# Kernel optimization log

Hardware: AMD Instinct MI355X
Metric: run time of the kernel (lower is better)

The kernel has to match this reference:

```python
import jax, jax.numpy as jnp
import numpy as np

B, T, D = 2, 2048, 2048
NH, NKV = 16, 4
HD = D // NH  # 128
BASE, TSL = 10000.0, 1024


def rotary_tables(T, hd, base=BASE, tsl=TSL):
    # Matches Rotary.forward with rd == hd (rd=0 in __init__ -> full head dim).
    ar = jnp.arange(0, hd, 2, dtype=jnp.float32) / hd
    if T <= tsl:
        inv = 1.0 / (base ** ar)
    else:
        # NTK-style rescale; note right-assoc exponent in original torch code:
        # 1/(base * (T/tsl) ** ((rd/(rd-2)) ** ar))
        inv = 1.0 / (base * jnp.power(T / tsl, jnp.power(hd / (hd - 2.0), ar)))
    f = jnp.outer(jnp.arange(T, dtype=jnp.float32), inv)  # [T, hd//2]
    cos = jnp.cos(f)[None, :, None, :]  # [1,T,1,hd//2]
    sin = jnp.sin(f)[None, :, None, :]
    return cos, sin


def apply_rope(x, cos, sin):
    # full-dim rope: split halves, rotate
    h = x.shape[-1] // 2
    x1, x2 = x[..., :h], x[..., h:]
    return jnp.concatenate((x1 * cos + x2 * sin, -x1 * sin + x2 * cos), axis=-1)


def rms_norm(x):
    eps = jnp.finfo(x.dtype).eps
    return x * jax.lax.rsqrt(jnp.mean(x * x, axis=-1, keepdims=True) + eps)


def setup_inputs() -> dict:
    key = jax.random.key(0)
    k0, k1, k2, k3, k4 = jax.random.split(key, 5)
    s = 0.02
    return {
        "x": jax.random.normal(k0, (B, T, D), jnp.float32),
        "qw": jax.random.normal(k1, (NH * HD, D), jnp.float32) * s,
        "kw": jax.random.normal(k2, (NKV * HD, D), jnp.float32) * s,
        "vw": jax.random.normal(k3, (NKV * HD, D), jnp.float32) * s,
        "ow": jax.random.normal(k4, (D, D), jnp.float32) * s,
        "qg": jnp.ones((NH,), jnp.float32),
    }


def reference(x, qw, kw, vw, ow, qg):
    Bx, Tx, Dx = x.shape
    q = (x @ qw.T).reshape(Bx, Tx, NH, HD)
    k = (x @ kw.T).reshape(Bx, Tx, NKV, HD)
    v = (x @ vw.T).reshape(Bx, Tx, NKV, HD)
    q = rms_norm(q)
    k = rms_norm(k)
    cos, sin = rotary_tables(Tx, HD)
    q = apply_rope(q, cos, sin) * qg[None, None, :, None]
    k = apply_rope(k, cos, sin)
    # GQA: repeat kv heads
    r = NH // NKV
    k = jnp.repeat(k, r, axis=2)  # [B,T,NH,HD]
    v = jnp.repeat(v, r, axis=2)
    scale = 1.0 / jnp.sqrt(jnp.asarray(HD, q.dtype))
    scores = jnp.einsum("bqhd,bkhd->bhqk", q, k) * scale  # [B,NH,T,T]
    causal = jnp.tril(jnp.ones((Tx, Tx), dtype=bool))
    scores = jnp.where(causal[None, None, :, :], scores, jnp.asarray(-jnp.inf, scores.dtype))
    attn = jax.nn.softmax(scores, axis=-1)
    y = jnp.einsum("bhqk,bkhd->bqhd", attn, v)  # [B,T,NH,HD]
    return y.reshape(Bx, Tx, Dx) @ ow.T
```

## Files before the change

kernel.cpp:

```cpp
#include <hip/hip_runtime.h>
#include <hip/hip_bf16.h>
#include <stdint.h>


typedef __attribute__((ext_vector_type(8))) short short8;
typedef __attribute__((ext_vector_type(4))) float f32x4;
typedef __attribute__((ext_vector_type(16))) float f32x16;

#define GLOAD16(gp, lp) \
  __builtin_amdgcn_global_load_lds((const __attribute__((address_space(1))) void*)(gp), \
                                   (__attribute__((address_space(3))) void*)(lp), 16, 0, 0)

#define BAR() do { asm volatile("" ::: "memory"); __builtin_amdgcn_s_barrier(); asm volatile("" ::: "memory"); } while (0)

__device__ __forceinline__ float bf2f(unsigned short u) {
  union { unsigned int i; float f; } v; v.i = ((unsigned int)u) << 16; return v.f;
}
__device__ __forceinline__ unsigned short f2bf(float f) {
  union { float fl; unsigned int i; } v; v.fl = f;
  unsigned int r = v.i + 0x7fffu + ((v.i >> 16) & 1u);
  return (unsigned short)(r >> 16);
}
__device__ __forceinline__ unsigned pk2(float a, float b) {
  return (unsigned)f2bf(a) | ((unsigned)f2bf(b) << 16);
}

__global__ __launch_bounds__(256) void prep_kernel(
    const float* __restrict__ x, const float* __restrict__ qw,
    const float* __restrict__ kw, const float* __restrict__ vw,
    const float* __restrict__ ow,
    unsigned short* __restrict__ xb, unsigned short* __restrict__ wqkv,
    unsigned short* __restrict__ owb, float* __restrict__ cost, float* __restrict__ sint) {
  const int NX = 2097152;
  const int NW = 1572864;
  const int NO = 1048576;
  const int NT = 131072;
  int tid = blockIdx.x * 256 + threadIdx.x;
  if (tid < NX) {
    float4 v = ((const float4*)x)[tid];
    uint2 o; o.x = pk2(v.x, v.y); o.y = pk2(v.z, v.w);
    ((uint2*)xb)[tid] = o;
  } else if (tid < NX + NW) {
    int i = tid - NX; int e = i * 4;
    const float* src = (e < 4194304) ? (qw + e)
                     : (e < 5242880) ? (kw + (e - 4194304))
                                     : (vw + (e - 5242880));
    float4 v = *(const float4*)src;
    uint2 o; o.x = pk2(v.x, v.y); o.y = pk2(v.z, v.w);
    ((uint2*)wqkv)[i] = o;
  } else if (tid < NX + NW + NO) {
    int i = tid - NX - NW;
    float4 v = ((const float4*)ow)[i];
    uint2 o; o.x = pk2(v.x, v.y); o.y = pk2(v.z, v.w);
    ((uint2*)owb)[i] = o;
  } else if (tid < NX + NW + NO + NT) {
    int i = tid - NX - NW - NO;
    int t = i >> 6, j = i & 63;
    float e = exp2f(0.02272008f * (float)j * (1.0f / 64.0f));
    float inv = 1.0f / (10000.0f * exp2f(e));
    float f = (float)t * inv;
    cost[i] = cosf(f);
    sint[i] = sinf(f);
  }
}

template <int IM, int NB, int OUTF>
__global__ __launch_bounds__(512) void gemm8ph(const unsigned short* __restrict__ A,
                                               const unsigned short* __restrict__ Bw,
                                               void* __restrict__ Cp,
                                               int MT, int NTn, int N, int K) {
  extern __shared__ char smc[];
  constexpr int S = IM * 8;
  constexpr int IQ = IM / 2;
  constexpr int JQ = NB / 128;
  constexpr int ASZ = IM * 2048;
  constexpr int BSZ = NB * 64;
  constexpr int DB = 2 * ASZ + 2 * BSZ;
  constexpr int AL = (IM * 128) / 512;
  constexpr int BL = NB / 128;
  constexpr int VMCN = AL + 2 * BL;
  const int tid = threadIdx.x;
  const int l = tid & 63, w = tid >> 6;
  const int lane_r = l & 15, lane_g = l >> 4;
  const int wr = w >> 2, wc = w & 3;

  int qch = (MT * NTn) >> 3;
  int orig = blockIdx.x;
  int wgid = (orig & 7) * qch + (orig >> 3);
  int by = wgid / NTn, bx = wgid - by * NTn;
  const int m0 = by * IM * 32, n0 = bx * NB;

  f32x4 acc[IM][2 * JQ];
#pragma unroll
  for (int i = 0; i < IM; ++i)
#pragma unroll
    for (int j = 0; j < 2 * JQ; ++j) acc[i][j] = {0.f, 0.f, 0.f, 0.f};

  const unsigned short* srcA[AL]; int ldA[AL];
#pragma unroll
  for (int t = 0; t < AL; ++t) {
    int idx = t * 512 + tid;
    int rc = idx >> 3, kc = idx & 7;
    int wrp = rc >= S ? 1 : 0, rr = rc & (S - 1);
    int row = wrp * 2 * S + rr;
    srcA[t] = A + (size_t)(m0 + row) * K + (kc ^ (rc & 7)) * 8;
    ldA[t] = idx * 16;
  }
  const unsigned short* srcB[BL]; int ldB[BL];
#pragma unroll
  for (int t = 0; t < BL; ++t) {
    int idx = t * 512 + tid;
    int rc = idx >> 3, kc = idx & 7;
    int g16 = rc >> 4;
    int nrow = (g16 / JQ) * (NB / 4) + (g16 % JQ) * 16 + (rc & 15);
    srcB[t] = Bw + (size_t)(n0 + nrow) * K + (kc ^ (rc & 7)) * 8;
    ldB[t] = idx * 16;
  }
  const int SK = S * K, JK = (NB / 8) * K;

  auto STA = [&](int kt, int ih, int dqb) {
    char* d = smc + dqb + ih * ASZ;
#pragma unroll
    for (int t = 0; t < AL; ++t) GLOAD16(srcA[t] + kt + ih * SK, d + ldA[t]);
  };
  auto STB = [&](int kt, int jh, int dqb) {
    char* d = smc + dqb + 2 * ASZ + jh * BSZ;
#pragma unroll
    for (int t = 0; t < BL; ++t) GLOAD16(srcB[t] + kt + jh * JK, d + ldB[t]);
  };

  int oA[IQ][2], oB[JQ][2];
#pragma unroll
  for (int iq = 0; iq < IQ; ++iq)
#pragma unroll
    for (int ks = 0; ks < 2; ++ks) {
      int rc = wr * S + iq * 16 + lane_r;
      oA[iq][ks] = rc * 128 + ((ks * 64 + lane_g * 16) ^ ((rc & 7) << 4));
    }
#pragma unroll
  for (int jj = 0; jj < JQ; ++jj)
#pragma unroll
    for (int ks = 0; ks < 2; ++ks) {
      int rc = wc * (NB / 8) + jj * 16 + lane_r;
      oB[jj][ks] = rc * 128 + ((ks * 64 + lane_g * 16) ^ ((rc & 7) << 4));
    }

#define VMC() asm volatile("s_waitcnt vmcnt(%0)" :: "i"(VMCN) : "memory")
#define VM0() asm volatile("s_waitcnt vmcnt(0)" ::: "memory")
#define MM(IH, JH, BR) do { \
    __builtin_amdgcn_s_setprio(1); \
    _Pragma("unroll") \
    for (int iq = 0; iq < IQ; ++iq) \
      _Pragma("unroll") \
      for (int jj = 0; jj < JQ; ++jj) \
        _Pragma("unroll") \
        for (int ks = 0; ks < 2; ++ks) \
          acc[(IH) * IQ + iq][(JH) * JQ + jj] = __builtin_amdgcn_mfma_f32_16x16x32_bf16( \
              af[iq][ks], BR[jj][ks], acc[(IH) * IQ + iq][(JH) * JQ + jj], 0, 0, 0); \
    __builtin_amdgcn_s_setprio(0); } while (0)

  const int NS = K >> 6;
  STA(0, 0, 0); STB(0, 0, 0); STB(0, 1, 0); STA(0, 1, 0);
  STA(64, 0, DB); STB(64, 0, DB); STB(64, 1, DB);
  VMC();
  BAR();

#pragma unroll 1
  for (int s = 0; s < NS; ++s) {
    const int dq = (s & 1) * DB, dn = DB - dq;
    const char* Ab = smc + dq;
    const char* Bb = Ab + 2 * ASZ;
    short8 af[IQ][2], b0[JQ][2], b1[JQ][2];
    if (s + 1 < NS) STA((s + 1) << 6, 1, dn);
#pragma unroll
    for (int iq = 0; iq < IQ; ++iq)
#pragma unroll
      for (int ks = 0; ks < 2; ++ks) af[iq][ks] = *(const short8*)(Ab + oA[iq][ks]);
#pragma unroll
    for (int jj = 0; jj < JQ; ++jj)
#pragma unroll
      for (int ks = 0; ks < 2; ++ks) b0[jj][ks] = *(const short8*)(Bb + oB[jj][ks]);
    MM(0, 0, b0);
    BAR();
    if (s + 2 < NS) STA((s + 2) << 6, 0, dq);
#pragma unroll
    for (int jj = 0; jj < JQ; ++jj)
#pragma unroll
      for (int ks = 0; ks < 2; ++ks) b1[jj][ks] = *(const short8*)(Bb + BSZ + oB[jj][ks]);
    MM(0, 1, b1);
    BAR();
    if (s + 2 < NS) STB((s + 2) << 6, 0, dq);
#pragma unroll
    for (int iq = 0; iq < IQ; ++iq)
#pragma unroll
      for (int ks = 0; ks < 2; ++ks) af[iq][ks] = *(const short8*)(Ab + ASZ + oA[iq][ks]);
    MM(1, 0, b0);
    BAR();
    if (s + 2 < NS) STB((s + 2) << 6, 1, dq);
    MM(1, 1, b1);
    if (s + 2 < NS) VMC(); else VM0();
    BAR();
  }
#undef VMC
#undef VM0
#undef MM

#pragma unroll
  for (int ih = 0; ih < 2; ++ih)
#pragma unroll
    for (int iq = 0; iq < IQ; ++iq) {
      int row = m0 + wr * 2 * S + ih * S + iq * 16 + lane_g * 4;
#pragma unroll
      for (int jh = 0; jh < 2; ++jh)
#pragma unroll
        for (int jj = 0; jj < JQ; ++jj) {
          int col = n0 + wc * (NB / 4) + jh * (NB / 8) + jj * 16 + lane_r;
#pragma unroll
          for (int r = 0; r < 4; ++r) {
            float v = acc[ih * IQ + iq][jh * JQ + jj][r];
            if (OUTF)
              ((float*)Cp)[(size_t)(row + r) * N + col] = v;
            else
              ((unsigned short*)Cp)[(size_t)(row + r) * N + col] = f2bf(v);
          }
        }
    }
}

__global__ __launch_bounds__(256) void normrope_vt_kernel(unsigned short* __restrict__ qkv,
                                                          const float* __restrict__ cost,
                                                          const float* __restrict__ sint,
                                                          const float* __restrict__ qg,
                                                          unsigned short* __restrict__ vtg) {
  __shared__ unsigned short tile[64][132];
  int bid = blockIdx.x;
  const int tid = threadIdx.x;
  if (bid < 20480) {
    const int l = tid & 63, w = tid >> 6;
    int row = bid * 4 + w;
    int tok = row / 20, hh = row - tok * 20;
    int t = tok & 2047;
    bool isq = hh < 16;
    int col0 = isq ? hh * 128 : 2048 + (hh - 16) * 128;
    unsigned short* p = qkv + (size_t)tok * 3072 + col0 + 2 * l;
    unsigned int u = *(const unsigned int*)p;
    float x0 = bf2f((unsigned short)(u & 0xffffu));
    float x1 = bf2f((unsigned short)(u >> 16));
    float ss = x0 * x0 + x1 * x1;
#pragma unroll
    for (int m = 1; m < 64; m <<= 1) ss += __shfl_xor(ss, m);
    float rn = rsqrtf(ss * (1.0f / 128.0f) + 1.1920928955078125e-07f);
    float n0 = x0 * rn, n1 = x1 * rn;
    float p0 = __shfl_xor(n0, 32);
    float p1 = __shfl_xor(n1, 32);
    int jj = (2 * l) & 63;
    float c0 = cost[t * 64 + jj], c1 = cost[t * 64 + jj + 1];
    float s0 = sint[t * 64 + jj], s1 = sint[t * 64 + jj + 1];
    float o0, o1;
    if (l < 32) { o0 = n0 * c0 + p0 * s0; o1 = n1 * c1 + p1 * s1; }
    else        { o0 = -p0 * s0 + n0 * c0; o1 = -p1 * s1 + n1 * c1; }
    if (isq) { float g = qg[hh] * 0.08838834764831845f * 1.4426950408889634f; o0 *= g; o1 *= g; }
    *(unsigned int*)p = pk2(o0, o1);
  } else {
    int bid2 = bid - 20480;
    int pan = bid2 & 7, tt = bid2 >> 3;
    int b = pan >> 2, kvh = pan & 3;
    int t0 = tt * 64;
    const unsigned short* src = qkv + ((size_t)(b * 2048 + t0)) * 3072 + 2560 + kvh * 128;
#pragma unroll
    for (int i = 0; i < 8; ++i) {
      int idx = i * 256 + tid;
      int row = idx >> 5, c4 = idx & 31;
      uint2 v = *(const uint2*)(src + (size_t)row * 3072 + c4 * 4);
      *(uint2*)&tile[row][c4 * 4] = v;
    }
    __syncthreads();
    unsigned short* dst = vtg + (size_t)pan * 262144 + t0;
#pragma unroll
    for (int i = 0; i < 8; ++i) {
      int idx = i * 256 + tid;
      int d = idx >> 4, tc = idx & 15;
      unsigned short a0 = tile[tc * 4 + 0][d], a1 = tile[tc * 4 + 1][d];
      unsigned short a2 = tile[tc * 4 + 2][d], a3 = tile[tc * 4 + 3][d];
      uint2 o; o.x = (unsigned)a0 | ((unsigned)a1 << 16);
      o.y = (unsigned)a2 | ((unsigned)a3 << 16);
      *(uint2*)(dst + (size_t)d * 2048 + tc * 4) = o;
    }
  }
}

__global__ __launch_bounds__(512) void attn_fa10(const unsigned short* __restrict__ qkv,
                                                 const unsigned short* __restrict__ vtg,
                                                 unsigned short* __restrict__ y) {
  extern __shared__ char smc[];
  const int tid = threadIdx.x;
  const int l = tid & 63, w = tid >> 6;
  const int lq = l & 31, hi = l >> 5;
  const int g = w & 3, hh = w >> 2;

  int n = blockIdx.x;
  int pan = n & 7;
  int b = pan >> 2, kvh = pan & 3;
  int idx2 = n >> 3;
  int h = kvh * 4 + (idx2 & 3);
  int pairIdx = idx2 >> 2;
  const size_t rowbase = (size_t)b * 2048;
  const unsigned short* kvK = qkv + rowbase * 3072;
  const unsigned short* vtp = vtg + (size_t)pan * 262144;

  int kg[4], vg[4], sl[4];
#pragma unroll
  for (int t = 0; t < 4; ++t) {
    int idx = t * 512 + tid;
    int row = idx >> 4, c = idx & 15, gc = c ^ (row & 7);
    kg[t] = row * 3072 + 2048 + kvh * 128 + gc * 8;
    vg[t] = row * 2048 + gc * 8;
    sl[t] = idx * 16;
  }
  const int swq = (lq & 7) << 4;
  const int krow = (hh * 64 + lq) * 256;
  int oxk[8];
#pragma unroll
  for (int ds = 0; ds < 8; ++ds) oxk[ds] = (ds * 32 + hi * 16) ^ swq;
  const int vrow = lq * 256;
  int oxv[4];
#pragma unroll
  for (int ksl = 0; ksl < 4; ++ksl) oxv[ksl] = (hh * 128 + ksl * 32 + hi * 16) ^ swq;
  const int mab = (g * 64 + l) * 256;
  const int mlb = 65536 + (g * 64 + l) * 8;
  const int lsw = (l & 7) << 4;

  auto STAGE = [&](int tile, int bufsel) {
    const unsigned short* srcK = kvK + (size_t)tile * 128 * 3072;
    const unsigned short* srcV = vtp + tile * 128;
    char* kd = smc + bufsel * 32768;
    char* vd = smc + 65536 + bufsel * 32768;
#pragma unroll
    for (int t = 0; t < 4; ++t) {
      GLOAD16(srcK + kg[t], kd + sl[t]);
      GLOAD16(srcV + vg[t], vd + sl[t]);
    }
  };

#pragma unroll 1
  for (int phase = 0; phase < 2; ++phase) {
    const int qt = phase ? pairIdx : 15 - pairIdx;
    const int q0 = qt * 128;
    const int nkb = qt + 1;
    const int wrow0 = q0 + g * 32;
    const int qrow = wrow0 + lq;

    STAGE(0, 0);
    short8 qf[8];
#pragma unroll
    for (int ds = 0; ds < 8; ++ds)
      qf[ds] = *(const short8*)(qkv + (rowbase + qrow) * 3072 + h * 128 + ds * 16 + hi * 8);

    f32x16 acc[4];
#pragma unroll
    for (int dt = 0; dt < 4; ++dt)
#pragma unroll
      for (int jj = 0; jj < 16; ++jj) acc[dt][jj] = 0.f;
    float mrun = -1e30f, lrun = 0.f;

    __syncthreads();

#pragma unroll 1
    for (int kb = 0; kb < nkb; ++kb) {
      const int cur = kb & 1;
      if (kb + 1 < nkb) STAGE(kb + 1, cur ^ 1);
      const int j0 = kb * 128;
      if (j0 + hh * 64 <= wrow0) {
        const int kbb = cur * 32768;
        const int vbb = 65536 + cur * 32768;
        f32x16 s0, s1;
#pragma unroll
        for (int jj = 0; jj < 16; ++jj) { s0[jj] = 0.f; s1[jj] = 0.f; }
        __builtin_amdgcn_s_setprio(1);
#pragma unroll
        for (int ds = 0; ds < 8; ++ds) {
          short8 kf = *(const short8*)(smc + kbb + krow + oxk[ds]);
          s0 = __builtin_amdgcn_mfma_f32_32x32x16_bf16(kf, qf[ds], s0, 0, 0, 0);
        }
#pragma unroll
        for (int ds = 0; ds < 8; ++ds) {
          short8 kf = *(const short8*)(smc + kbb + 8192 + krow + oxk[ds]);
          s1 = __builtin_amdgcn_mfma_f32_32x32x16_bf16(kf, qf[ds], s1, 0, 0, 0);
        }
        __builtin_amdgcn_s_setprio(0);
        const int rq = qrow - j0 - hh * 64;
        if (rq < 63) {
#pragma unroll
          for (int jj = 0; jj < 16; ++jj) {
            int kl = (jj & 3) + 8 * (jj >> 2) + 4 * hi;
            s0[jj] = (kl > rq) ? -1e30f : s0[jj];
            s1[jj] = (kl + 32 > rq) ? -1e30f : s1[jj];
          }
        }
        float pmax = s0[0];
#pragma unroll
        for (int jj = 0; jj < 16; ++jj) pmax = fmaxf(pmax, fmaxf(s0[jj], s1[jj]));
        pmax = fmaxf(pmax, __shfl_xor(pmax, 32));
        if (!__all(pmax - mrun <= 11.5f)) {
          float mn = fmaxf(mrun, pmax);
          float corr = exp2f(mrun - mn);
          lrun *= corr;
#pragma unroll
          for (int dt = 0; dt < 4; ++dt)
#pragma unroll
            for (int jj = 0; jj < 16; ++jj) acc[dt][jj] *= corr;
          mrun = mn;
        }
        float rs = 0.f;
#pragma unroll
        for (int jj = 0; jj < 16; ++jj) {
          s0[jj] = exp2f(s0[jj] - mrun); rs += s0[jj];
          s1[jj] = exp2f(s1[jj] - mrun); rs += s1[jj];
        }
        rs += __shfl_xor(rs, 32);
        lrun += rs;
        unsigned r0[8], r1[8];
#pragma unroll
        for (int j = 0; j < 4; ++j) {
          asm("v_cvt_pk_bf16_f32 %0, %1, %2" : "=v"(r0[2 * j]) : "v"(s0[4 * j]), "v"(s0[4 * j + 1]));
          asm("v_cvt_pk_bf16_f32 %0, %1, %2" : "=v"(r0[2 * j + 1]) : "v"(s0[4 * j + 2]), "v"(s0[4 * j + 3]));
          asm("v_cvt_pk_bf16_f32 %0, %1, %2" : "=v"(r1[2 * j]) : "v"(s1[4 * j]), "v"(s1[4 * j + 1]));
          asm("v_cvt_pk_bf16_f32 %0, %1, %2" : "=v"(r1[2 * j + 1]) : "v"(s1[4 * j + 2]), "v"(s1[4 * j + 3]));
        }
        __builtin_amdgcn_s_setprio(1);
#pragma unroll
        for (int ksl = 0; ksl < 4; ++ksl) {
          unsigned* rr = (ksl < 2) ? r0 : r1;
          int kk = ksl & 1;
          unsigned w0 = rr[4 * kk], w2 = rr[4 * kk + 2];
          asm("v_permlane32_swap_b32 %0, %1" : "+v"(w0), "+v"(w2));
          unsigned w1 = rr[4 * kk + 1], w3 = rr[4 * kk + 3];
          asm("v_permlane32_swap_b32 %0, %1" : "+v"(w1), "+v"(w3));
          union { unsigned u[4]; short8 s8; } pu;
          pu.u[0] = w0; pu.u[1] = w1; pu.u[2] = w2; pu.u[3] = w3;
          short8 pf = pu.s8;
#pragma unroll
          for (int dt = 0; dt < 4; ++dt) {
            short8 vf = *(const short8*)(smc + vbb + dt * 8192 + vrow + oxv[ksl]);
            acc[dt] = __builtin_amdgcn_mfma_f32_32x32x16_bf16(vf, pf, acc[dt], 0, 0, 0);
          }
        }
        __builtin_amdgcn_s_setprio(0);
      }
      __syncthreads();
    }
    if (hh) {
#pragma unroll
      for (int dt = 0; dt < 4; ++dt)
#pragma unroll
        for (int q4 = 0; q4 < 4; ++q4) {
          f32x4 v = {acc[dt][4 * q4], acc[dt][4 * q4 + 1], acc[dt][4 * q4 + 2], acc[dt][4 * q4 + 3]};
          *(f32x4*)(smc + mab + ((dt * 64 + q4 * 16) ^ lsw)) = v;
        }
      *(float2*)(smc + mlb) = {mrun, lrun};
    }
    __syncthreads();
    if (!hh) {
      float2 ml = *(const float2*)(smc + mlb);
      float mx = fmaxf(mrun, ml.x);
      float sc0 = exp2f(mrun - mx), sc1 = exp2f(ml.x - mx);
      lrun = lrun * sc0 + ml.y * sc1;
#pragma unroll
      for (int dt = 0; dt < 4; ++dt)
#pragma unroll
        for (int q4 = 0; q4 < 4; ++q4) {
          f32x4 v = *(const f32x4*)(smc + mab + ((dt * 64 + q4 * 16) ^ lsw));
#pragma unroll
          for (int r = 0; r < 4; ++r)
            acc[dt][4 * q4 + r] = acc[dt][4 * q4 + r] * sc0 + v[r] * sc1;
        }
    }
    __syncthreads();
    if (!hh) {
      float linv = 1.0f / lrun;
      unsigned short* yrow = y + (rowbase + qrow) * 2048 + h * 128;
#pragma unroll
      for (int dt = 0; dt < 4; ++dt)
#pragma unroll
        for (int m = 0; m < 4; ++m) {
          uint2 o;
          o.x = pk2(acc[dt][4 * m] * linv, acc[dt][4 * m + 1] * linv);
          o.y = pk2(acc[dt][4 * m + 2] * linv, acc[dt][4 * m + 3] * linv);
          *(uint2*)(yrow + dt * 32 + m * 8 + hi * 4) = o;
        }
    }
  }
}

extern "C" void kernel_launch(void* const* d_in, const int* in_sizes, int n_in,
                              void* d_out, int out_size, void* d_ws, size_t ws_size,
                              hipStream_t stream) {
  (void)in_sizes; (void)n_in; (void)out_size; (void)ws_size;
  const float* x  = (const float*)d_in[0];
  const float* qw = (const float*)d_in[1];
  const float* kw = (const float*)d_in[2];
  const float* vw = (const float*)d_in[3];
  const float* ow = (const float*)d_in[4];
  const float* qg = (const float*)d_in[5];

  char* ws = (char*)d_ws;
  unsigned short* xb   = (unsigned short*)(ws + 0);
  unsigned short* vtg  = (unsigned short*)(ws + 0);
  unsigned short* wqkv = (unsigned short*)(ws + 16777216);
  unsigned short* owb  = (unsigned short*)(ws + 29360128);
  unsigned short* qkvb = (unsigned short*)(ws + 37748736);
  unsigned short* y    = (unsigned short*)(ws + 62914560);
  float* cost          = (float*)(ws + 79691776);
  float* sint          = (float*)(ws + 80216064);

  prep_kernel<<<18944, 256, 0, stream>>>(x, qw, kw, vw, ow, xb, wqkv, owb, cost, sint);
  gemm8ph<4, 384, 0><<<256, 512, 131072, stream>>>(xb, wqkv, qkvb, 32, 8, 3072, 2048);
  normrope_vt_kernel<<<20736, 256, 0, stream>>>(qkvb, cost, sint, qg, vtg);
  attn_fa10<<<256, 512, 131072, stream>>>(qkvb, vtg, y);
  gemm8ph<4, 256, 1><<<256, 512, 98304, stream>>>(y, owb, d_out, 32, 8, 2048, 2048);
}
```

Measured before the change: 186.5 us.

## Split attention KV tile across four wave groups with tree combine

The attention kernel goes from 512 to 1024 threads per block. Each of four key-quarter wave groups now handles 32 keys of every 128-key tile instead of two halves handling 64, so each wave carries one score accumulator instead of two. Partial softmax states are merged through a two-level shared-memory reduction, which adds extra barriers and spill/combine passes and raises LDS use slightly. The intent is more waves per CU to hide latency and lower per-wave register pressure, at the cost of more synchronisation and combine work.

```diff
diff --git a/kernel.cpp b/kernel.cpp
--- a/kernel.cpp
+++ b/kernel.cpp
@@ -289,14 +289,14 @@
   }
 }
 
-__global__ __launch_bounds__(512) void attn_fa10(const unsigned short* __restrict__ qkv,
-                                                 const unsigned short* __restrict__ vtg,
-                                                 unsigned short* __restrict__ y) {
+__global__ __launch_bounds__(1024, 4) void attn_fa11(const unsigned short* __restrict__ qkv,
+                                                     const unsigned short* __restrict__ vtg,
+                                                     unsigned short* __restrict__ y) {
   extern __shared__ char smc[];
   const int tid = threadIdx.x;
   const int l = tid & 63, w = tid >> 6;
   const int lq = l & 31, hi = l >> 5;
-  const int g = w & 3, hh = w >> 2;
+  const int g = w & 3, kq = w >> 2;
 
   int n = blockIdx.x;
   int pan = n & 7;
@@ -308,26 +308,25 @@
   const unsigned short* kvK = qkv + rowbase * 3072;
   const unsigned short* vtp = vtg + (size_t)pan * 262144;
 
-  int kg[4], vg[4], sl[4];
-#pragma unroll
-  for (int t = 0; t < 4; ++t) {
-    int idx = t * 512 + tid;
+  int kg[2], vg[2], sl[2];
+#pragma unroll
+  for (int t = 0; t < 2; ++t) {
+    int idx = t * 1024 + tid;
     int row = idx >> 4, c = idx & 15, gc = c ^ (row & 7);
     kg[t] = row * 3072 + 2048 + kvh * 128 + gc * 8;
     vg[t] = row * 2048 + gc * 8;
     sl[t] = idx * 16;
   }
   const int swq = (lq & 7) << 4;
-  const int krow = (hh * 64 + lq) * 256;
+  const int krow = (kq * 32 + lq) * 256;
   int oxk[8];
 #pragma unroll
   for (int ds = 0; ds < 8; ++ds) oxk[ds] = (ds * 32 + hi * 16) ^ swq;
   const int vrow = lq * 256;
-  int oxv[4];
-#pragma unroll
-  for (int ksl = 0; ksl < 4; ++ksl) oxv[ksl] = (hh * 128 + ksl * 32 + hi * 16) ^ swq;
-  const int mab = (g * 64 + l) * 256;
-  const int mlb = 65536 + (g * 64 + l) * 8;
+  int oxv[2];
+#pragma unroll
+  for (int ksl = 0; ksl < 2; ++ksl) oxv[ksl] = (kq * 64 + ksl * 32 + hi * 16) ^ swq;
+  const int mslot = (g * 64 + l) * 256;
   const int lsw = (l & 7) << 4;
 
   auto STAGE = [&](int tile, int bufsel) {
@@ -336,7 +335,7 @@
     char* kd = smc + bufsel * 32768;
     char* vd = smc + 65536 + bufsel * 32768;
 #pragma unroll
-    for (int t = 0; t < 4; ++t) {
+    for (int t = 0; t < 2; ++t) {
       GLOAD16(srcK + kg[t], kd + sl[t]);
       GLOAD16(srcV + vg[t], vd + sl[t]);
     }
@@ -350,6 +349,7 @@
     const int wrow0 = q0 + g * 32;
     const int qrow = wrow0 + lq;
 
+    __syncthreads();
     STAGE(0, 0);
     short8 qf[8];
 #pragma unroll
@@ -370,36 +370,30 @@
       const int cur = kb & 1;
       if (kb + 1 < nkb) STAGE(kb + 1, cur ^ 1);
       const int j0 = kb * 128;
-      if (j0 + hh * 64 <= wrow0) {
+      if (j0 + kq * 32 <= wrow0) {
         const int kbb = cur * 32768;
         const int vbb = 65536 + cur * 32768;
-        f32x16 s0, s1;
-#pragma unroll
-        for (int jj = 0; jj < 16; ++jj) { s0[jj] = 0.f; s1[jj] = 0.f; }
+        f32x16 s;
+#pragma unroll
+        for (int jj = 0; jj < 16; ++jj) s[jj] = 0.f;
         __builtin_amdgcn_s_setprio(1);
 #pragma unroll
         for (int ds = 0; ds < 8; ++ds) {
           short8 kf = *(const short8*)(smc + kbb + krow + oxk[ds]);
-          s0 = __builtin_amdgcn_mfma_f32_32x32x16_bf16(kf, qf[ds], s0, 0, 0, 0);
-        }
-#pragma unroll
-        for (int ds = 0; ds < 8; ++ds) {
-          short8 kf = *(const short8*)(smc + kbb + 8192 + krow + oxk[ds]);
-          s1 = __builtin_amdgcn_mfma_f32_32x32x16_bf16(kf, qf[ds], s1, 0, 0, 0);
+          s = __builtin_amdgcn_mfma_f32_32x32x16_bf16(kf, qf[ds], s, 0, 0, 0);
         }
         __builtin_amdgcn_s_setprio(0);
-        const int rq = qrow - j0 - hh * 64;
-        if (rq < 63) {
+        const int rq = qrow - j0 - kq * 32;
+        if (rq < 31) {
 #pragma unroll
           for (int jj = 0; jj < 16; ++jj) {
             int kl = (jj & 3) + 8 * (jj >> 2) + 4 * hi;
-            s0[jj] = (kl > rq) ? -1e30f : s0[jj];
-            s1[jj] = (kl + 32 > rq) ? -1e30f : s1[jj];
+            s[jj] = (kl > rq) ? -1e30f : s[jj];
           }
         }
-        float pmax = s0[0];
-#pragma unroll
-        for (int jj = 0; jj < 16; ++jj) pmax = fmaxf(pmax, fmaxf(s0[jj], s1[jj]));
+        float pmax = s[0];
+#pragma unroll
+        for (int jj = 1; jj < 16; ++jj) pmax = fmaxf(pmax, s[jj]);
         pmax = fmaxf(pmax, __shfl_xor(pmax, 32));
         if (!__all(pmax - mrun <= 11.5f)) {
           float mn = fmaxf(mrun, pmax);
@@ -413,28 +407,21 @@
         }
         float rs = 0.f;
 #pragma unroll
-        for (int jj = 0; jj < 16; ++jj) {
-          s0[jj] = exp2f(s0[jj] - mrun); rs += s0[jj];
-          s1[jj] = exp2f(s1[jj] - mrun); rs += s1[jj];
-        }
+        for (int jj = 0; jj < 16; ++jj) { s[jj] = exp2f(s[jj] - mrun); rs += s[jj]; }
         rs += __shfl_xor(rs, 32);
         lrun += rs;
-        unsigned r0[8], r1[8];
+        unsigned r[8];
 #pragma unroll
         for (int j = 0; j < 4; ++j) {
-          asm("v_cvt_pk_bf16_f32 %0, %1, %2" : "=v"(r0[2 * j]) : "v"(s0[4 * j]), "v"(s0[4 * j + 1]));
-          asm("v_cvt_pk_bf16_f32 %0, %1, %2" : "=v"(r0[2 * j + 1]) : "v"(s0[4 * j + 2]), "v"(s0[4 * j + 3]));
-          asm("v_cvt_pk_bf16_f32 %0, %1, %2" : "=v"(r1[2 * j]) : "v"(s1[4 * j]), "v"(s1[4 * j + 1]));
-          asm("v_cvt_pk_bf16_f32 %0, %1, %2" : "=v"(r1[2 * j + 1]) : "v"(s1[4 * j + 2]), "v"(s1[4 * j + 3]));
+          asm("v_cvt_pk_bf16_f32 %0, %1, %2" : "=v"(r[2 * j]) : "v"(s[4 * j]), "v"(s[4 * j + 1]));
+          asm("v_cvt_pk_bf16_f32 %0, %1, %2" : "=v"(r[2 * j + 1]) : "v"(s[4 * j + 2]), "v"(s[4 * j + 3]));
         }
         __builtin_amdgcn_s_setprio(1);
 #pragma unroll
-        for (int ksl = 0; ksl < 4; ++ksl) {
-          unsigned* rr = (ksl < 2) ? r0 : r1;
-          int kk = ksl & 1;
-          unsigned w0 = rr[4 * kk], w2 = rr[4 * kk + 2];
+        for (int ksl = 0; ksl < 2; ++ksl) {
+          unsigned w0 = r[4 * ksl], w2 = r[4 * ksl + 2];
           asm("v_permlane32_swap_b32 %0, %1" : "+v"(w0), "+v"(w2));
-          unsigned w1 = rr[4 * kk + 1], w3 = rr[4 * kk + 3];
+          unsigned w1 = r[4 * ksl + 1], w3 = r[4 * ksl + 3];
           asm("v_permlane32_swap_b32 %0, %1" : "+v"(w1), "+v"(w3));
           union { unsigned u[4]; short8 s8; } pu;
           pu.u[0] = w0; pu.u[1] = w1; pu.u[2] = w2; pu.u[3] = w3;
@@ -449,34 +436,44 @@
       }
       __syncthreads();
     }
-    if (hh) {
+
+    auto SPILL = [&](int accbase, int mlbase) {
 #pragma unroll
       for (int dt = 0; dt < 4; ++dt)
 #pragma unroll
         for (int q4 = 0; q4 < 4; ++q4) {
           f32x4 v = {acc[dt][4 * q4], acc[dt][4 * q4 + 1], acc[dt][4 * q4 + 2], acc[dt][4 * q4 + 3]};
-          *(f32x4*)(smc + mab + ((dt * 64 + q4 * 16) ^ lsw)) = v;
-        }
-      *(float2*)(smc + mlb) = {mrun, lrun};
-    }
-    __syncthreads();
-    if (!hh) {
-      float2 ml = *(const float2*)(smc + mlb);
+          *(f32x4*)(smc + accbase + mslot + ((dt * 64 + q4 * 16) ^ lsw)) = v;
+        }
+      *(float2*)(smc + mlbase + (g * 64 + l) * 8) = {mrun, lrun};
+    };
+    auto COMBINE = [&](int accbase, int mlbase) {
+      float2 ml = *(const float2*)(smc + mlbase + (g * 64 + l) * 8);
       float mx = fmaxf(mrun, ml.x);
       float sc0 = exp2f(mrun - mx), sc1 = exp2f(ml.x - mx);
       lrun = lrun * sc0 + ml.y * sc1;
+      mrun = mx;
 #pragma unroll
       for (int dt = 0; dt < 4; ++dt)
 #pragma unroll
         for (int q4 = 0; q4 < 4; ++q4) {
-          f32x4 v = *(const f32x4*)(smc + mab + ((dt * 64 + q4 * 16) ^ lsw));
-#pragma unroll
-          for (int r = 0; r < 4; ++r)
-            acc[dt][4 * q4 + r] = acc[dt][4 * q4 + r] * sc0 + v[r] * sc1;
-        }
-    }
+          f32x4 v = *(const f32x4*)(smc + accbase + mslot + ((dt * 64 + q4 * 16) ^ lsw));
+#pragma unroll
+          for (int r2 = 0; r2 < 4; ++r2)
+            acc[dt][4 * q4 + r2] = acc[dt][4 * q4 + r2] * sc0 + v[r2] * sc1;
+        }
+    };
+
+    if (kq == 1) SPILL(0, 131072);
+    if (kq == 3) SPILL(65536, 133120);
     __syncthreads();
-    if (!hh) {
+    if (kq == 0) COMBINE(0, 131072);
+    if (kq == 2) COMBINE(65536, 133120);
+    __syncthreads();
+    if (kq == 2) SPILL(0, 131072);
+    __syncthreads();
+    if (kq == 0) {
+      COMBINE(0, 131072);
       float linv = 1.0f / lrun;
       unsigned short* yrow = y + (rowbase + qrow) * 2048 + h * 128;
 #pragma unroll
@@ -516,6 +513,6 @@
   prep_kernel<<<18944, 256, 0, stream>>>(x, qw, kw, vw, ow, xb, wqkv, owb, cost, sint);
   gemm8ph<4, 384, 0><<<256, 512, 131072, stream>>>(xb, wqkv, qkvb, 32, 8, 3072, 2048);
   normrope_vt_kernel<<<20736, 256, 0, stream>>>(qkvb, cost, sint, qg, vtg);
-  attn_fa10<<<256, 512, 131072, stream>>>(qkvb, vtg, y);
+  attn_fa11<<<256, 1024, 135168, stream>>>(qkvb, vtg, y);
   gemm8ph<4, 256, 1><<<256, 512, 98304, stream>>>(y, owb, d_out, 32, 8, 2048, 2048);
 }
```

Result: slower. 255.1 us (+36.8%).
